# Kernel optimization log

Measured on AMD Instinct MI355X. Metric: run time of the kernel, lower is better.

Reference implementation:

```python
import jax, jax.numpy as jnp
import numpy as np

B, T, D = 4, 2048, 1024
H = 16
DK = D // H

def setup_inputs() -> dict:
    key = jax.random.key(0)
    k1, k2, k3, k4, k5 = jax.random.split(key, 5)
    s = 1.0 / np.sqrt(D)
    return {
        "x": jax.random.normal(k1, (B, T, D), dtype=jnp.float32),
        # torch Linear convention: weight [out, in], y = x @ W.T + b
        "W_qkv": jax.random.uniform(k2, (3 * D, D), jnp.float32, -s, s),
        "b_qkv": jax.random.uniform(k3, (3 * D,), jnp.float32, -s, s),
        "W_proj": jax.random.uniform(k4, (D, D), jnp.float32, -s, s),
        "b_proj": jax.random.uniform(k5, (D,), jnp.float32, -s, s),
    }

def reference(x, W_qkv, b_qkv, W_proj, b_proj):
    Bx, Tx, C = x.shape
    qkv = x @ W_qkv.T + b_qkv                      # [B,T,3D]
    qkv = qkv.reshape(Bx, Tx, 3, H, DK)
    qkv = jnp.transpose(qkv, (2, 0, 3, 1, 4))      # [3,B,H,T,dk]
    q, k, v = qkv[0], qkv[1], qkv[2]
    att = jnp.einsum('bhqd,bhkd->bhqk', q, k) / np.sqrt(DK)
    causal = jnp.tril(jnp.ones((Tx, Tx), dtype=bool))
    att = jnp.where(causal[None, None], att, -jnp.inf)
    att = jax.nn.softmax(att, axis=-1)
    out = jnp.einsum('bhqk,bhkd->bhqd', att, v)    # [B,H,T,dk]
    out = jnp.transpose(out, (0, 2, 1, 3)).reshape(Bx, Tx, C)
    return out @ W_proj.T + b_proj
```

## Files before the change

kernel.cpp:

```cpp
#include <hip/hip_runtime.h>

typedef unsigned short ushort_t;
typedef __attribute__((ext_vector_type(8))) short short8;
typedef __attribute__((ext_vector_type(4))) float f32x4;

#define DEV __device__ __forceinline__

constexpr int B_ = 4, T_ = 2048, D_ = 1024, H_ = 16;
constexpr int M_ = B_ * T_;
constexpr float LOG2E_ = 1.4426950408889634f;

DEV ushort_t f2bf(float f) {
  union { float f; unsigned u; } c; c.f = f;
  unsigned u = c.u;
  return (ushort_t)((u + 0x7fffu + ((u >> 16) & 1u)) >> 16);
}
DEV float bf2f(ushort_t b) {
  union { unsigned u; float f; } c; c.u = ((unsigned)b) << 16;
  return c.f;
}
DEV unsigned cvt_pk_bf16(float lo, float hi) {
  unsigned r;
  asm("v_cvt_pk_bf16_f32 %0, %1, %2" : "=v"(r) : "v"(lo), "v"(hi));
  return r;
}

DEV void gload_lds16(const void* g, void* l) {
  __builtin_amdgcn_global_load_lds(
      (const __attribute__((address_space(1))) void*)g,
      (__attribute__((address_space(3))) void*)l, 16, 0, 0);
}

__global__ void __launch_bounds__(256) f2bf3_kernel(
    const float* __restrict__ a, ushort_t* __restrict__ oa, int na4,
    const float* __restrict__ b, ushort_t* __restrict__ ob, int nb4,
    const float* __restrict__ c, ushort_t* __restrict__ oc, int nc4) {
  int stride = gridDim.x * blockDim.x;
  int ntot = na4 + nb4 + nc4;
  for (int i = blockIdx.x * blockDim.x + threadIdx.x; i < ntot; i += stride) {
    const float* src;
    ushort_t* dst;
    int j = i;
    if (j < na4) {
      src = a; dst = oa;
    } else if (j < na4 + nb4) {
      j -= na4; src = b; dst = ob;
    } else {
      j -= na4 + nb4; src = c; dst = oc;
    }
    float4 v = reinterpret_cast<const float4*>(src)[j];
    ushort4 o;
    o.x = f2bf(v.x); o.y = f2bf(v.y); o.z = f2bf(v.z); o.w = f2bf(v.w);
    reinterpret_cast<ushort4*>(dst)[j] = o;
  }
}

template <bool OUT_BF16>
__global__ void __launch_bounds__(256) gemm_bt(
    const ushort_t* __restrict__ A, const ushort_t* __restrict__ Bw,
    const float* __restrict__ bias, void* __restrict__ Cout,
    ushort_t* __restrict__ VT, int M, int N, int K, int ldc) {
  __shared__ __align__(16) ushort_t lA[128 * 64];
  __shared__ __align__(16) ushort_t lB[128 * 64];
  const int tid = threadIdx.x;
  const int lane = tid & 63;
  const int w = tid >> 6;
  const int wm = w >> 1, wn = w & 1;
  const int r0 = lane & 15;
  const int p = lane >> 4;
  const int g8 = p * 8;
  const int rg = p * 4;

  const int tn2 = N >> 8;
  const int G = (M >> 7) * tn2;
  const int lin = blockIdx.x;
  const int cpx = G >> 3;
  const int swz = (lin & 7) * cpx + (lin >> 3);
  const int m0 = (swz / tn2) * 128;
  const int pn = swz % tn2;

  const int sf0 = tid * 8;

  for (int t = 0; t < 2; ++t) {
    const int n0 = (pn * 2 + t) * 128;

    f32x4 acc[4][4] = {};

    for (int k0 = 0; k0 < K; k0 += 64) {
#pragma unroll
      for (int it = 0; it < 4; ++it) {
        int f = it * 2048 + sf0;
        int row = f >> 6;
        int lch = ((f >> 3) & 7) ^ (row & 7);
        gload_lds16(A + (size_t)(m0 + row) * K + k0 + lch * 8, &lA[f]);
        gload_lds16(Bw + (size_t)(n0 + row) * K + k0 + lch * 8, &lB[f]);
      }
      __syncthreads();
      __builtin_amdgcn_s_setprio(1);
#pragma unroll
      for (int kc = 0; kc < 2; ++kc) {
        const int ch = (kc * 4 + p) ^ (r0 & 7);
        short8 aF[4], bF[4];
#pragma unroll
        for (int mi = 0; mi < 4; ++mi)
          aF[mi] = *(const short8*)&lA[(wm * 64 + mi * 16 + r0) * 64 + ch * 8];
#pragma unroll
        for (int ni = 0; ni < 4; ++ni)
          bF[ni] = *(const short8*)&lB[(wn * 64 + ni * 16 + r0) * 64 + ch * 8];
#pragma unroll
        for (int mi = 0; mi < 4; ++mi)
#pragma unroll
          for (int ni = 0; ni < 4; ++ni)
            acc[mi][ni] = __builtin_amdgcn_mfma_f32_16x16x32_bf16(
                aF[mi], bF[ni], acc[mi][ni], 0, 0, 0);
      }
      __builtin_amdgcn_s_setprio(0);
      __syncthreads();
    }

    const bool vpath = (VT != nullptr) && (n0 >= 2048);
    if (vpath) {
#pragma unroll
      for (int mi = 0; mi < 4; ++mi)
#pragma unroll
        for (int ni = 0; ni < 4; ++ni) {
          int n = n0 + wn * 64 + ni * 16 + r0;
          float bv = bias[n];
          int vcol = n - 2048;
          int hh = vcol >> 6, dd = vcol & 63;
          int m = m0 + wm * 64 + mi * 16 + rg;
          int bb = m >> 11, tt = m & 2047;
          ushort4 o;
          o.x = f2bf(acc[mi][ni][0] + bv);
          o.y = f2bf(acc[mi][ni][1] + bv);
          o.z = f2bf(acc[mi][ni][2] + bv);
          o.w = f2bf(acc[mi][ni][3] + bv);
          *reinterpret_cast<ushort4*>(
              &VT[((size_t)((bb << 4) + hh) * 64 + dd) * (size_t)T_ + tt]) = o;
        }
    } else {
#pragma unroll
      for (int mi = 0; mi < 4; ++mi)
#pragma unroll
        for (int ni = 0; ni < 4; ++ni) {
          int n = n0 + wn * 64 + ni * 16 + r0;
          float bv = bias[n];
#pragma unroll
          for (int r = 0; r < 4; ++r) {
            int m = m0 + wm * 64 + mi * 16 + rg + r;
            float v = acc[mi][ni][r] + bv;
            if (OUT_BF16)
              ((ushort_t*)Cout)[(size_t)m * ldc + n] = f2bf(v);
            else
              ((float*)Cout)[(size_t)m * ldc + n] = v;
          }
        }
    }
  }
}

__global__ void __launch_bounds__(256, 4) attn_kernel(
    const ushort_t* __restrict__ qk, const ushort_t* __restrict__ Vt,
    ushort_t* __restrict__ O) {
  __shared__ __align__(16) ushort_t lK[2][64 * 64];
  __shared__ __align__(16) ushort_t lVT[2][64 * 64];
  __shared__ __align__(16) ushort_t lP[4][16 * 64];

  const int tid = threadIdx.x;
  const int lane = tid & 63;
  const int w = tid >> 6;
  const int r0 = lane & 15;
  const int p = lane >> 4;
  const int g8 = p * 8;
  const int rg = p * 4;

  const int lin = (int)blockIdx.y * 16 + (int)blockIdx.x;
  const int xcd = lin & 7;
  const int chunk = lin >> 3;
  const int bh = xcd * 8 + (chunk >> 4);
  const int pair = chunk & 15;

  const int b = bh >> 4, h = bh & 15;
  const float QSC = 0.125f * LOG2E_;

  const short8 bOne = {0x3F80, 0x3F80, 0x3F80, 0x3F80,
                       0x3F80, 0x3F80, 0x3F80, 0x3F80};

  ushort_t* lPw = &lP[w][0];

  const int f0 = tid * 8;
  const int row0 = f0 >> 6;
  const int lch0 = ((f0 >> 3) & 7) ^ (row0 & 7);
  const int f1 = 2048 + tid * 8;
  const int row1 = f1 >> 6;
  const int lch1 = ((f1 >> 3) & 7) ^ (row1 & 7);

  const int qb1 = pair;
  const int qb2 = 31 - pair;
  const int q1 = qb1 * 64 + w * 16;
  const int q2 = qb2 * 64 + w * 16;

  short8 aQ1[2], aQ2[2];
#pragma unroll
  for (int kc = 0; kc < 2; ++kc) {
    short8 raw1 = *(const short8*)(qk + (size_t)(b * T_ + q1 + r0) * 2048 +
                                   h * 64 + kc * 32 + g8);
    short8 raw2 = *(const short8*)(qk + (size_t)(b * T_ + q2 + r0) * 2048 +
                                   h * 64 + kc * 32 + g8);
    short8 s1, s2;
#pragma unroll
    for (int j = 0; j < 4; ++j) {
      unsigned pk1 = cvt_pk_bf16(bf2f((ushort_t)raw1[2 * j]) * QSC,
                                 bf2f((ushort_t)raw1[2 * j + 1]) * QSC);
      unsigned pk2 = cvt_pk_bf16(bf2f((ushort_t)raw2[2 * j]) * QSC,
                                 bf2f((ushort_t)raw2[2 * j + 1]) * QSC);
      s1[2 * j] = (short)(ushort_t)pk1;
      s1[2 * j + 1] = (short)(ushort_t)(pk1 >> 16);
      s2[2 * j] = (short)(ushort_t)pk2;
      s2[2 * j + 1] = (short)(ushort_t)(pk2 >> 16);
    }
    aQ1[kc] = s1;
    aQ2[kc] = s2;
  }

  f32x4 accO1[4] = {}, accO2[4] = {};
  f32x4 accL1 = {}, accL2 = {};

  {
    const ushort_t* kb = qk + (size_t)(b * T_) * 2048 + 1024 + h * 64;
    const ushort_t* vb = Vt + (size_t)bh * 64 * (size_t)T_;
    gload_lds16(kb + (size_t)row0 * 2048 + lch0 * 8, &lK[0][f0]);
    gload_lds16(kb + (size_t)row1 * 2048 + lch1 * 8, &lK[0][f1]);
    gload_lds16(vb + (size_t)row0 * T_ + lch0 * 8, &lVT[0][f0]);
    gload_lds16(vb + (size_t)row1 * T_ + lch1 * 8, &lVT[0][f1]);
  }
  int cur = 0;

  auto procPV = [&](f32x4* sA, const ushort_t* bufV, f32x4* accO,
                    f32x4& accL) {
#pragma unroll
    for (int ni = 0; ni < 4; ++ni) {
      float p0 = exp2f(sA[ni][0]);
      float p1 = exp2f(sA[ni][1]);
      float p2 = exp2f(sA[ni][2]);
      float p3 = exp2f(sA[ni][3]);
      unsigned lo = cvt_pk_bf16(p0, p1);
      unsigned hi = cvt_pk_bf16(p2, p3);
      int col = ni * 16 + r0;
#pragma unroll
      for (int r = 0; r < 4; ++r) {
        int rowp = rg + r;
        ushort_t hw = (r == 0)   ? (ushort_t)lo
                      : (r == 1) ? (ushort_t)(lo >> 16)
                      : (r == 2) ? (ushort_t)hi
                                 : (ushort_t)(hi >> 16);
        lPw[rowp * 64 + (col ^ ((rowp & 7) << 3))] = hw;
      }
    }
    __builtin_amdgcn_s_setprio(1);
#pragma unroll
    for (int kc = 0; kc < 2; ++kc) {
      int pch = (kc * 4 + p) ^ (r0 & 7);
      short8 aP = *(const short8*)&lPw[r0 * 64 + pch * 8];
      accL = __builtin_amdgcn_mfma_f32_16x16x32_bf16(aP, bOne, accL, 0, 0, 0);
#pragma unroll
      for (int ni = 0; ni < 4; ++ni) {
        int row = ni * 16 + r0;
        int ch = (kc * 4 + p) ^ (row & 7);
        short8 bV = *(const short8*)&bufV[row * 64 + ch * 8];
        accO[ni] =
            __builtin_amdgcn_mfma_f32_16x16x32_bf16(aP, bV, accO[ni], 0, 0, 0);
      }
    }
    __builtin_amdgcn_s_setprio(0);
  };

  for (int kt = 0; kt <= qb2; ++kt) {
    __syncthreads();

    if (kt < qb2) {
      const ushort_t* kb =
          qk + (size_t)(b * T_ + (kt + 1) * 64) * 2048 + 1024 + h * 64;
      const ushort_t* vb = Vt + (size_t)bh * 64 * (size_t)T_ + (kt + 1) * 64;
      ushort_t* dK = &lK[cur ^ 1][0];
      ushort_t* dV = &lVT[cur ^ 1][0];
      gload_lds16(kb + (size_t)row0 * 2048 + lch0 * 8, dK + f0);
      gload_lds16(kb + (size_t)row1 * 2048 + lch1 * 8, dK + f1);
      gload_lds16(vb + (size_t)row0 * T_ + lch0 * 8, dV + f0);
      gload_lds16(vb + (size_t)row1 * T_ + lch1 * 8, dV + f1);
    }

    const ushort_t* bufK = &lK[cur][0];
    const ushort_t* bufV = &lVT[cur][0];
    const bool act1 = (kt <= qb1);

    f32x4 sA2[4];
#pragma unroll
    for (int ni = 0; ni < 4; ++ni)
      sA2[ni] = f32x4{-16.f, -16.f, -16.f, -16.f};
    __builtin_amdgcn_s_setprio(1);
#pragma unroll
    for (int kc = 0; kc < 2; ++kc)
#pragma unroll
      for (int ni = 0; ni < 4; ++ni) {
        int row = ni * 16 + r0;
        int ch = (kc * 4 + p) ^ (row & 7);
        short8 bK = *(const short8*)&bufK[row * 64 + ch * 8];
        sA2[ni] =
            __builtin_amdgcn_mfma_f32_16x16x32_bf16(aQ2[kc], bK, sA2[ni], 0, 0, 0);
      }
    __builtin_amdgcn_s_setprio(0);
    if (kt == qb2) {
#pragma unroll
      for (int ni = 0; ni < 4; ++ni) {
        if (ni > w) {
#pragma unroll
          for (int r = 0; r < 4; ++r) sA2[ni][r] = -1e30f;
        } else if (ni == w) {
#pragma unroll
          for (int r = 0; r < 4; ++r)
            if (r0 > rg + r) sA2[ni][r] = -1e30f;
        }
      }
    }
    procPV(sA2, bufV, accO2, accL2);

    if (act1) {
      f32x4 sA1[4];
#pragma unroll
      for (int ni = 0; ni < 4; ++ni)
        sA1[ni] = f32x4{-16.f, -16.f, -16.f, -16.f};
      __builtin_amdgcn_s_setprio(1);
#pragma unroll
      for (int kc = 0; kc < 2; ++kc)
#pragma unroll
        for (int ni = 0; ni < 4; ++ni) {
          int row = ni * 16 + r0;
          int ch = (kc * 4 + p) ^ (row & 7);
          short8 bK = *(const short8*)&bufK[row * 64 + ch * 8];
          sA1[ni] = __builtin_amdgcn_mfma_f32_16x16x32_bf16(aQ1[kc], bK,
                                                            sA1[ni], 0, 0, 0);
        }
      __builtin_amdgcn_s_setprio(0);
      if (kt == qb1) {
#pragma unroll
        for (int ni = 0; ni < 4; ++ni) {
          if (ni > w) {
#pragma unroll
            for (int r = 0; r < 4; ++r) sA1[ni][r] = -1e30f;
          } else if (ni == w) {
#pragma unroll
            for (int r = 0; r < 4; ++r)
              if (r0 > rg + r) sA1[ni][r] = -1e30f;
          }
        }
      }
      procPV(sA1, bufV, accO1, accL1);
    }

    cur ^= 1;
  }

#pragma unroll
  for (int ni = 0; ni < 4; ++ni)
#pragma unroll
    for (int r = 0; r < 4; ++r) {
      int d = h * 64 + ni * 16 + r0;
      float v1 = accO1[ni][r] / accL1[r];
      float v2 = accO2[ni][r] / accL2[r];
      O[(size_t)(b * T_ + q1 + rg + r) * 1024 + d] = f2bf(v1);
      O[(size_t)(b * T_ + q2 + rg + r) * 1024 + d] = f2bf(v2);
    }
}

extern "C" void kernel_launch(void* const* d_in, const int* in_sizes, int n_in,
                              void* d_out, int out_size, void* d_ws, size_t ws_size,
                              hipStream_t stream) {
  const float* x = (const float*)d_in[0];
  const float* Wqkv = (const float*)d_in[1];
  const float* bqkv = (const float*)d_in[2];
  const float* Wproj = (const float*)d_in[3];
  const float* bproj = (const float*)d_in[4];
  float* out = (float*)d_out;

  ushort_t* xb = (ushort_t*)d_ws;
  ushort_t* wqkvb = xb + (size_t)M_ * D_;
  ushort_t* wprojb = wqkvb + (size_t)3 * D_ * D_;
  ushort_t* qkb = wprojb + (size_t)D_ * D_;
  ushort_t* Vt = qkb + (size_t)M_ * 2048;
  ushort_t* Ob = Vt + (size_t)M_ * D_;

  f2bf3_kernel<<<2048, 256, 0, stream>>>(
      x, xb, M_ * D_ / 4,
      Wqkv, wqkvb, 3 * D_ * D_ / 4,
      Wproj, wprojb, D_ * D_ / 4);

  gemm_bt<true><<<768, 256, 0, stream>>>(
      xb, wqkvb, bqkv, qkb, Vt, M_, 3 * D_, D_, 2048);

  attn_kernel<<<dim3(16, 64), 256, 0, stream>>>(qkb, Vt, Ob);

  gemm_bt<false><<<256, 256, 0, stream>>>(
      Ob, wprojb, bproj, out, nullptr, M_, D_, D_, D_);
}
```

Before: 196.7 us.

## Replace GEMM with 256x128 tile, 512-thread, triple-buffered LDS pipeline

The GEMM kernel now uses 512-thread blocks computing a 256x128 output tile instead of looping over two 128x128 tiles. LDS is triple-buffered, so global-to-LDS loads for tile k+2 are issued while tile k is computed, with a partial vmcnt wait and raw barriers replacing the full syncthreads after each load. This is meant to hide load latency and increase A reuse, at the cost of far more LDS (144 KB), which limits occupancy. The prefetch wraps around and reloads early tiles redundantly at the end.

```diff
diff --git a/kernel.cpp b/kernel.cpp
--- a/kernel.cpp
+++ b/kernel.cpp
@@ -56,106 +56,137 @@
 }
 
 template <bool OUT_BF16>
-__global__ void __launch_bounds__(256) gemm_bt(
+__global__ void __launch_bounds__(512) gemm256(
     const ushort_t* __restrict__ A, const ushort_t* __restrict__ Bw,
     const float* __restrict__ bias, void* __restrict__ Cout,
     ushort_t* __restrict__ VT, int M, int N, int K, int ldc) {
-  __shared__ __align__(16) ushort_t lA[128 * 64];
-  __shared__ __align__(16) ushort_t lB[128 * 64];
+  __shared__ __align__(16) ushort_t lA[3][256 * 64];
+  __shared__ __align__(16) ushort_t lB[3][128 * 64];
   const int tid = threadIdx.x;
   const int lane = tid & 63;
-  const int w = tid >> 6;
-  const int wm = w >> 1, wn = w & 1;
+  const int wid = tid >> 6;
+  const int wm = wid >> 1, wn = wid & 1;
   const int r0 = lane & 15;
   const int p = lane >> 4;
-  const int g8 = p * 8;
   const int rg = p * 4;
 
-  const int tn2 = N >> 8;
-  const int G = (M >> 7) * tn2;
+  const int nbn = N >> 7;
+  const int G = (M >> 8) * nbn;
   const int lin = blockIdx.x;
   const int cpx = G >> 3;
   const int swz = (lin & 7) * cpx + (lin >> 3);
-  const int m0 = (swz / tn2) * 128;
-  const int pn = swz % tn2;
-
-  const int sf0 = tid * 8;
-
-  for (int t = 0; t < 2; ++t) {
-    const int n0 = (pn * 2 + t) * 128;
-
-    f32x4 acc[4][4] = {};
-
-    for (int k0 = 0; k0 < K; k0 += 64) {
-#pragma unroll
-      for (int it = 0; it < 4; ++it) {
-        int f = it * 2048 + sf0;
-        int row = f >> 6;
-        int lch = ((f >> 3) & 7) ^ (row & 7);
-        gload_lds16(A + (size_t)(m0 + row) * K + k0 + lch * 8, &lA[f]);
-        gload_lds16(Bw + (size_t)(n0 + row) * K + k0 + lch * 8, &lB[f]);
-      }
-      __syncthreads();
-      __builtin_amdgcn_s_setprio(1);
-#pragma unroll
-      for (int kc = 0; kc < 2; ++kc) {
-        const int ch = (kc * 4 + p) ^ (r0 & 7);
-        short8 aF[4], bF[4];
-#pragma unroll
-        for (int mi = 0; mi < 4; ++mi)
-          aF[mi] = *(const short8*)&lA[(wm * 64 + mi * 16 + r0) * 64 + ch * 8];
+  const int m0 = (swz / nbn) << 8;
+  const int n0 = (swz % nbn) << 7;
+
+  const int NKT = K >> 6;
+
+  auto stage = [&](int kt, int slot) {
+#pragma unroll
+    for (int rnd = 0; rnd < 4; ++rnd) {
+      int f = rnd * 4096 + tid * 8;
+      int row = f >> 6;
+      int sch = ((f >> 3) & 7) ^ (row & 7);
+      gload_lds16(A + (size_t)(m0 + row) * K + kt * 64 + sch * 8,
+                  &lA[slot][f]);
+    }
+#pragma unroll
+    for (int rnd = 0; rnd < 2; ++rnd) {
+      int f = rnd * 4096 + tid * 8;
+      int row = f >> 6;
+      int sch = ((f >> 3) & 7) ^ (row & 7);
+      gload_lds16(Bw + (size_t)(n0 + row) * K + kt * 64 + sch * 8,
+                  &lB[slot][f]);
+    }
+  };
+
+  f32x4 acc[4][4] = {};
+
+  stage(0, 0);
+  stage(1, 1);
+
+  for (int kt = 0; kt < NKT; ++kt) {
+    int skt = kt + 2;
+    if (skt >= NKT) skt -= NKT;
+    stage(skt, (kt + 2) % 3);
+
+    asm volatile("s_waitcnt vmcnt(12)" ::: "memory");
+    __builtin_amdgcn_sched_barrier(0);
+    asm volatile("s_barrier" ::: "memory");
+    __builtin_amdgcn_sched_barrier(0);
+
+    const ushort_t* bA = &lA[kt % 3][0];
+    const ushort_t* bB = &lB[kt % 3][0];
+
+    short8 aF[2][4], bF[2][4];
+#pragma unroll
+    for (int kc = 0; kc < 2; ++kc)
+#pragma unroll
+      for (int mi = 0; mi < 4; ++mi) {
+        int row = wm * 64 + mi * 16 + r0;
+        int ch = (kc * 4 + p) ^ (row & 7);
+        aF[kc][mi] = *(const short8*)&bA[row * 64 + ch * 8];
+      }
+#pragma unroll
+    for (int kc = 0; kc < 2; ++kc)
+#pragma unroll
+      for (int ni = 0; ni < 4; ++ni) {
+        int row = wn * 64 + ni * 16 + r0;
+        int ch = (kc * 4 + p) ^ (row & 7);
+        bF[kc][ni] = *(const short8*)&bB[row * 64 + ch * 8];
+      }
+
+    __builtin_amdgcn_s_setprio(1);
+#pragma unroll
+    for (int kc = 0; kc < 2; ++kc)
+#pragma unroll
+      for (int mi = 0; mi < 4; ++mi)
 #pragma unroll
         for (int ni = 0; ni < 4; ++ni)
-          bF[ni] = *(const short8*)&lB[(wn * 64 + ni * 16 + r0) * 64 + ch * 8];
-#pragma unroll
-        for (int mi = 0; mi < 4; ++mi)
-#pragma unroll
-          for (int ni = 0; ni < 4; ++ni)
-            acc[mi][ni] = __builtin_amdgcn_mfma_f32_16x16x32_bf16(
-                aF[mi], bF[ni], acc[mi][ni], 0, 0, 0);
-      }
-      __builtin_amdgcn_s_setprio(0);
-      __syncthreads();
-    }
-
-    const bool vpath = (VT != nullptr) && (n0 >= 2048);
-    if (vpath) {
-#pragma unroll
-      for (int mi = 0; mi < 4; ++mi)
-#pragma unroll
-        for (int ni = 0; ni < 4; ++ni) {
-          int n = n0 + wn * 64 + ni * 16 + r0;
-          float bv = bias[n];
-          int vcol = n - 2048;
-          int hh = vcol >> 6, dd = vcol & 63;
-          int m = m0 + wm * 64 + mi * 16 + rg;
-          int bb = m >> 11, tt = m & 2047;
-          ushort4 o;
-          o.x = f2bf(acc[mi][ni][0] + bv);
-          o.y = f2bf(acc[mi][ni][1] + bv);
-          o.z = f2bf(acc[mi][ni][2] + bv);
-          o.w = f2bf(acc[mi][ni][3] + bv);
-          *reinterpret_cast<ushort4*>(
-              &VT[((size_t)((bb << 4) + hh) * 64 + dd) * (size_t)T_ + tt]) = o;
+          acc[mi][ni] = __builtin_amdgcn_mfma_f32_16x16x32_bf16(
+              aF[kc][mi], bF[kc][ni], acc[mi][ni], 0, 0, 0);
+    __builtin_amdgcn_s_setprio(0);
+
+    asm volatile("s_barrier" ::: "memory");
+    __builtin_amdgcn_sched_barrier(0);
+  }
+
+  const bool vpath = (VT != nullptr) && (n0 >= 2048);
+  if (vpath) {
+#pragma unroll
+    for (int mi = 0; mi < 4; ++mi)
+#pragma unroll
+      for (int ni = 0; ni < 4; ++ni) {
+        int n = n0 + wn * 64 + ni * 16 + r0;
+        float bv = bias[n];
+        int vcol = n - 2048;
+        int hh = vcol >> 6, dd = vcol & 63;
+        int m = m0 + wm * 64 + mi * 16 + rg;
+        int bb = m >> 11, tt = m & 2047;
+        ushort4 o;
+        o.x = f2bf(acc[mi][ni][0] + bv);
+        o.y = f2bf(acc[mi][ni][1] + bv);
+        o.z = f2bf(acc[mi][ni][2] + bv);
+        o.w = f2bf(acc[mi][ni][3] + bv);
+        *reinterpret_cast<ushort4*>(
+            &VT[((size_t)((bb << 4) + hh) * 64 + dd) * (size_t)T_ + tt]) = o;
+      }
+  } else {
+#pragma unroll
+    for (int mi = 0; mi < 4; ++mi)
+#pragma unroll
+      for (int ni = 0; ni < 4; ++ni) {
+        int n = n0 + wn * 64 + ni * 16 + r0;
+        float bv = bias[n];
+#pragma unroll
+        for (int r = 0; r < 4; ++r) {
+          int m = m0 + wm * 64 + mi * 16 + rg + r;
+          float v = acc[mi][ni][r] + bv;
+          if (OUT_BF16)
+            ((ushort_t*)Cout)[(size_t)m * ldc + n] = f2bf(v);
+          else
+            ((float*)Cout)[(size_t)m * ldc + n] = v;
         }
-    } else {
-#pragma unroll
-      for (int mi = 0; mi < 4; ++mi)
-#pragma unroll
-        for (int ni = 0; ni < 4; ++ni) {
-          int n = n0 + wn * 64 + ni * 16 + r0;
-          float bv = bias[n];
-#pragma unroll
-          for (int r = 0; r < 4; ++r) {
-            int m = m0 + wm * 64 + mi * 16 + rg + r;
-            float v = acc[mi][ni][r] + bv;
-            if (OUT_BF16)
-              ((ushort_t*)Cout)[(size_t)m * ldc + n] = f2bf(v);
-            else
-              ((float*)Cout)[(size_t)m * ldc + n] = v;
-          }
-        }
-    }
+      }
   }
 }
 
@@ -395,11 +426,11 @@
       Wqkv, wqkvb, 3 * D_ * D_ / 4,
       Wproj, wprojb, D_ * D_ / 4);
 
-  gemm_bt<true><<<768, 256, 0, stream>>>(
+  gemm256<true><<<768, 512, 0, stream>>>(
       xb, wqkvb, bqkv, qkb, Vt, M_, 3 * D_, D_, 2048);
 
   attn_kernel<<<dim3(16, 64), 256, 0, stream>>>(qkb, Vt, Ob);
 
-  gemm_bt<false><<<256, 256, 0, stream>>>(
+  gemm256<false><<<256, 512, 0, stream>>>(
       Ob, wprojb, bproj, out, nullptr, M_, D_, D_, D_);
 }
```

Result: faster. 184.4 us, median of 4 (-6.3%).
